# Kernel tuning notes

Measured on AMD Instinct MI355X. Metric: run time of the kernel, lower is better.

The kernel has to match this reference:

```python
import jax, jax.numpy as jnp
import numpy as np

B, H, C_LEN, Q_LEN = 64, 128, 1024, 128


def setup_inputs() -> dict:
    key = jax.random.key(0)
    k1, k2, k3 = jax.random.split(key, 3)
    context = jax.random.normal(k1, (B, H, C_LEN), dtype=jnp.float32)
    question = jax.random.normal(k2, (B, H, Q_LEN), dtype=jnp.float32)
    lim = np.sqrt(1.0 / H)
    w = jax.random.uniform(k3, (3 * H,), dtype=jnp.float32, minval=-lim, maxval=lim)
    return {"context": context, "question": question, "w": w}


def reference(context, question, w):
    # context: (B, H, C), question: (B, H, Q); w: (3H,) with cat order (q, c, cq)
    h = w.shape[0] // 3
    w_q, w_c, w_cq = w[:h], w[h:2 * h], w[2 * h:]
    c = jnp.transpose(context, (0, 2, 1))   # (B, C, H)
    q = jnp.transpose(question, (0, 2, 1))  # (B, Q, H)
    # trilinear similarity s[b,i,j] = c_i.w_c + q_j.w_q + (c_i*w_cq).q_j  -> (B, C, Q)
    s = (c @ w_c)[:, :, None] + (q @ w_q)[:, None, :] \
        + jnp.einsum('bih,bjh->bij', c * w_cq, q)
    # original applies softmax over dim=1 (context axis) for BOTH s1 and s2
    s1 = jax.nn.softmax(s, axis=1)           # (B, C, Q)
    a = jnp.einsum('bij,bjh->bih', s1, q)    # (B, C, H)
    l = jnp.einsum('bij,bkj->bik', s1, s1)   # (B, C, C)
    b = jnp.einsum('bik,bkh->bih', l, c)     # (B, C, H)
    out = jnp.concatenate([c, a, c * a, c * b], axis=2)  # (B, C, 4H)
    # dropout disabled (drop_prob=0) for deterministic reference
    return jnp.transpose(out, (0, 2, 1))     # (B, 4H, C)
```

## Files before the change

### kernel.cpp

```cpp
#include <hip/hip_runtime.h>

#define BB 64
#define HH 128
#define CC 1024
#define QQ 128

typedef unsigned short u16;
typedef unsigned int u32;
using bf16x8 = __attribute__((ext_vector_type(8))) short;
using f32x4 = __attribute__((ext_vector_type(4))) float;

#define MFMA16(a, b, c) __builtin_amdgcn_mfma_f32_16x16x32_bf16(a, b, c, 0, 0, 0)

__device__ __forceinline__ float lo2f(u32 u) {
  union { float f; u32 i; } v; v.i = u << 16; return v.f;
}
__device__ __forceinline__ float hi2f(u32 u) {
  union { float f; u32 i; } v; v.i = u & 0xFFFF0000u; return v.f;
}
__device__ __forceinline__ u16 f2b(float f) {
  union { float f; u32 i; } v; v.f = f;
  u32 r = v.i + 0x7FFFu + ((v.i >> 16) & 1u);
  return (u16)(r >> 16);
}
__device__ __forceinline__ u32 pack_hi2(float a, float b) {
  return (__float_as_uint(a) >> 16) | (__float_as_uint(b) & 0xFFFF0000u);
}
__device__ __forceinline__ u32 pack_lo2(float a, float b) {
  float ra = a - __uint_as_float(__float_as_uint(a) & 0xFFFF0000u);
  float rb = b - __uint_as_float(__float_as_uint(b) & 0xFFFF0000u);
  return (__float_as_uint(ra) >> 16) | (__float_as_uint(rb) & 0xFFFF0000u);
}

__device__ __forceinline__ void stage16(const float* __restrict__ p,
                                        u16* dhi, u16* dlo) {
  float4 a0 = *(const float4*)p;
  float4 a1 = *(const float4*)(p + 4);
  float4 a2 = *(const float4*)(p + 8);
  float4 a3 = *(const float4*)(p + 12);
  uint4 h0 = {pack_hi2(a0.x, a0.y), pack_hi2(a0.z, a0.w),
              pack_hi2(a1.x, a1.y), pack_hi2(a1.z, a1.w)};
  uint4 h1 = {pack_hi2(a2.x, a2.y), pack_hi2(a2.z, a2.w),
              pack_hi2(a3.x, a3.y), pack_hi2(a3.z, a3.w)};
  uint4 l0 = {pack_lo2(a0.x, a0.y), pack_lo2(a0.z, a0.w),
              pack_lo2(a1.x, a1.y), pack_lo2(a1.z, a1.w)};
  uint4 l1 = {pack_lo2(a2.x, a2.y), pack_lo2(a2.z, a2.w),
              pack_lo2(a3.x, a3.y), pack_lo2(a3.z, a3.w)};
  *(uint4*)dhi = h0;
  *(uint4*)(dhi + 8) = h1;
  *(uint4*)dlo = l0;
  *(uint4*)(dlo + 8) = l1;
}

__global__ __launch_bounds__(512) void k1_s_softmax(
    const float* __restrict__ ctx, const float* __restrict__ qst,
    const float* __restrict__ w, u16* __restrict__ s1ws,
    u16* __restrict__ s1tb) {
  const int b = blockIdx.x;
  const int j0 = blockIdx.y * 16;
  const int tid = threadIdx.x;
  const float* cb = ctx + (size_t)b * HH * CC;
  const float* qb = qst + (size_t)b * HH * QQ;

  float dotv[16][2];
  float qwq[16];
  float cwc[2] = {0.f, 0.f};
#pragma unroll
  for (int jj = 0; jj < 16; ++jj) {
    qwq[jj] = 0.f;
    dotv[jj][0] = dotv[jj][1] = 0.f;
  }

  for (int h = 0; h < HH; ++h) {
    const float2 cv = *(const float2*)(cb + (size_t)h * CC + tid * 2);
    float c0 = cv.x, c1 = cv.y;
    float wqv = w[h], wcv = w[HH + h], wcqv = w[2 * HH + h];
    cwc[0] += c0 * wcv; cwc[1] += c1 * wcv;
    float t0 = c0 * wcqv, t1 = c1 * wcqv;
    const float4* qrow = (const float4*)(qb + (size_t)h * QQ + j0);
    float4 q0 = qrow[0], q1 = qrow[1], q2 = qrow[2], q3 = qrow[3];
    float qv[16] = {q0.x, q0.y, q0.z, q0.w, q1.x, q1.y, q1.z, q1.w,
                    q2.x, q2.y, q2.z, q2.w, q3.x, q3.y, q3.z, q3.w};
#pragma unroll
    for (int jj = 0; jj < 16; ++jj) {
      qwq[jj] += qv[jj] * wqv;
      dotv[jj][0] += t0 * qv[jj];
      dotv[jj][1] += t1 * qv[jj];
    }
  }
#pragma unroll
  for (int jj = 0; jj < 16; ++jj) {
    float base = qwq[jj];
    dotv[jj][0] += cwc[0] + base;
    dotv[jj][1] += cwc[1] + base;
  }

  __shared__ float red[16 * 512];
  __shared__ float red2[16 * 32];
  __shared__ float bc[16];
  const int rj = tid >> 5, rs = tid & 31;

#pragma unroll
  for (int jj = 0; jj < 16; ++jj)
    red[jj * 512 + tid] = fmaxf(dotv[jj][0], dotv[jj][1]);
  __syncthreads();
  {
    float m = red[rj * 512 + rs * 16];
#pragma unroll
    for (int g = 1; g < 16; ++g) m = fmaxf(m, red[rj * 512 + rs * 16 + g]);
    red2[rj * 32 + rs] = m;
  }
  __syncthreads();
  if (tid < 16) {
    float m = red2[tid * 32];
#pragma unroll
    for (int g = 1; g < 32; ++g) m = fmaxf(m, red2[tid * 32 + g]);
    bc[tid] = m;
  }
  __syncthreads();

#pragma unroll
  for (int jj = 0; jj < 16; ++jj) {
    float mj = bc[jj];
    float e0 = __expf(dotv[jj][0] - mj);
    float e1 = __expf(dotv[jj][1] - mj);
    dotv[jj][0] = e0; dotv[jj][1] = e1;
    red[jj * 512 + tid] = e0 + e1;
  }
  __syncthreads();
  {
    float s = 0.f;
#pragma unroll
    for (int g = 0; g < 16; ++g) s += red[rj * 512 + rs * 16 + g];
    red2[rj * 32 + rs] = s;
  }
  __syncthreads();
  if (tid < 16) {
    float s = 0.f;
#pragma unroll
    for (int g = 0; g < 32; ++g) s += red2[tid * 32 + g];
    bc[tid] = 1.0f / s;
  }
  __syncthreads();

#pragma unroll
  for (int jj = 0; jj < 16; ++jj) {
    float inv = bc[jj];
    dotv[jj][0] *= inv;
    dotv[jj][1] *= inv;
  }
  u16* srow = s1ws + ((size_t)b * QQ + j0) * CC + tid * 2;
#pragma unroll
  for (int jj = 0; jj < 16; ++jj) {
    u32 pk = (u32)f2b(dotv[jj][0]) | ((u32)f2b(dotv[jj][1]) << 16);
    *(u32*)(srow + (size_t)jj * CC) = pk;
  }
  u16* stb = s1tb + (size_t)b * (16 * 1024 * 8);
  const int jg0 = j0 >> 3;
#pragma unroll
  for (int g = 0; g < 2; ++g) {
#pragma unroll
    for (int rr = 0; rr < 2; ++rr) {
      const int o = g * 8;
      uint4 v;
      v.x = (u32)f2b(dotv[o + 0][rr]) | ((u32)f2b(dotv[o + 1][rr]) << 16);
      v.y = (u32)f2b(dotv[o + 2][rr]) | ((u32)f2b(dotv[o + 3][rr]) << 16);
      v.z = (u32)f2b(dotv[o + 4][rr]) | ((u32)f2b(dotv[o + 5][rr]) << 16);
      v.w = (u32)f2b(dotv[o + 6][rr]) | ((u32)f2b(dotv[o + 7][rr]) << 16);
      *(uint4*)(stb + ((size_t)(jg0 + g) * 1024 + (tid * 2 + rr)) * 8) = v;
    }
  }
}

__global__ __launch_bounds__(256) void k2_t(
    const float* __restrict__ ctx, const u16* __restrict__ s1ws,
    float* __restrict__ tT) {
  const int b = blockIdx.x;
  const int h0 = (blockIdx.y >> 1) * 32;
  const int j0 = (blockIdx.y & 1) * 64;
  const int tid = threadIdx.x;
  const int lane = tid & 63;
  const int wv = tid >> 6;
  const int l15 = lane & 15, l4 = lane >> 4;

  __shared__ u16 sHi[32 * 136];
  __shared__ u16 sLo[32 * 136];

  f32x4 acc[2];
  acc[0] = 0.f; acc[1] = 0.f;

  const float* cb = ctx + ((size_t)b * HH + h0) * CC;
  const u16* sb = s1ws + ((size_t)b * QQ + j0 + wv * 16 + l15) * CC;
  const int srow = tid >> 3;
  const int scol = (tid & 7) * 16;

  for (int k0 = 0; k0 < CC; k0 += 128) {
    __syncthreads();
    stage16(cb + (size_t)srow * CC + k0 + scol,
            &sHi[srow * 136 + scol], &sLo[srow * 136 + scol]);
    __syncthreads();
#pragma unroll
    for (int kk = 0; kk < 4; ++kk) {
      bf16x8 bf = *(const bf16x8*)(sb + k0 + kk * 32 + l4 * 8);
#pragma unroll
      for (int ht = 0; ht < 2; ++ht) {
        const int ar = (ht * 16 + l15) * 136 + kk * 32 + l4 * 8;
        bf16x8 ah = *(const bf16x8*)&sHi[ar];
        bf16x8 al = *(const bf16x8*)&sLo[ar];
        acc[ht] = MFMA16(ah, bf, acc[ht]);
        acc[ht] = MFMA16(al, bf, acc[ht]);
      }
    }
  }
  float* tb = tT + (size_t)b * HH * QQ;
#pragma unroll
  for (int ht = 0; ht < 2; ++ht)
#pragma unroll
    for (int r = 0; r < 4; ++r)
      tb[(size_t)(h0 + ht * 16 + l4 * 4 + r) * QQ + j0 + wv * 16 + l15] =
          acc[ht][r];
}

__global__ __launch_bounds__(256, 2) void k3_out(
    const float* __restrict__ ctx, const float* __restrict__ qst,
    const u16* __restrict__ s1tb, const float* __restrict__ tT,
    float* __restrict__ out) {
  const int b = blockIdx.x;
  const int i0 = blockIdx.y * 128;
  const int tid = threadIdx.x;
  const int lane = tid & 63;
  const int wv = tid >> 6;
  const int l15 = lane & 15, l4 = lane >> 4;

  __shared__ u16 qHi[128 * 40], qLo[128 * 40];
  __shared__ u16 tHi[128 * 40], tLo[128 * 40];

  f32x4 accA[8][2], accB[8][2];
#pragma unroll
  for (int it = 0; it < 8; ++it)
#pragma unroll
    for (int ht = 0; ht < 2; ++ht) { accA[it][ht] = 0.f; accB[it][ht] = 0.f; }

  const u16* stb = s1tb + (size_t)b * (16 * 1024 * 8);
  const float* qb = qst + (size_t)b * HH * QQ;
  const float* tb = tT + (size_t)b * HH * QQ;
  const int srow = tid >> 1;
  const int scol = (tid & 1) * 16;

  for (int ks = 0; ks < 4; ++ks) {
    const int jb = ks * 32;
    __syncthreads();
    stage16(qb + (size_t)srow * QQ + jb + scol,
            &qHi[srow * 40 + scol], &qLo[srow * 40 + scol]);
    stage16(tb + (size_t)srow * QQ + jb + scol,
            &tHi[srow * 40 + scol], &tLo[srow * 40 + scol]);
    __syncthreads();
    bf16x8 qh[2], ql[2], th[2], tl[2];
#pragma unroll
    for (int ht = 0; ht < 2; ++ht) {
      const int ar = (wv * 32 + ht * 16 + l15) * 40 + l4 * 8;
      qh[ht] = *(const bf16x8*)&qHi[ar];
      ql[ht] = *(const bf16x8*)&qLo[ar];
      th[ht] = *(const bf16x8*)&tHi[ar];
      tl[ht] = *(const bf16x8*)&tLo[ar];
    }
#pragma unroll
    for (int half = 0; half < 2; ++half) {
      bf16x8 bfr[4];
#pragma unroll
      for (int t4 = 0; t4 < 4; ++t4) {
        const int it = half * 4 + t4;
        bfr[t4] = *(const bf16x8*)(stb +
            ((size_t)(ks * 4 + l4) * 1024 + i0 + it * 16 + l15) * 8);
      }
#pragma unroll
      for (int t4 = 0; t4 < 4; ++t4) {
        const int it = half * 4 + t4;
#pragma unroll
        for (int ht = 0; ht < 2; ++ht) {
          accA[it][ht] = MFMA16(qh[ht], bfr[t4], accA[it][ht]);
          accA[it][ht] = MFMA16(ql[ht], bfr[t4], accA[it][ht]);
          accB[it][ht] = MFMA16(th[ht], bfr[t4], accB[it][ht]);
          accB[it][ht] = MFMA16(tl[ht], bfr[t4], accB[it][ht]);
        }
      }
    }
  }

  const float* cb = ctx + (size_t)b * HH * CC;
  float* ob = out + (size_t)b * 4 * HH * CC;
#pragma unroll
  for (int it = 0; it < 8; ++it) {
    const int ii = i0 + it * 16 + l15;
#pragma unroll
    for (int ht = 0; ht < 2; ++ht) {
#pragma unroll
      for (int r = 0; r < 4; ++r) {
        const int h = wv * 32 + ht * 16 + l4 * 4 + r;
        const size_t base = (size_t)h * CC + ii;
        const float cv = cb[base];
        const float av = accA[it][ht][r];
        const float bv = accB[it][ht][r];
        ob[base] = cv;
        ob[(size_t)HH * CC + base] = av;
        ob[(size_t)2 * HH * CC + base] = cv * av;
        ob[(size_t)3 * HH * CC + base] = cv * bv;
      }
    }
  }
}

extern "C" void kernel_launch(void* const* d_in, const int* in_sizes, int n_in,
                              void* d_out, int out_size, void* d_ws, size_t ws_size,
                              hipStream_t stream) {
  const float* ctx = (const float*)d_in[0];
  const float* qst = (const float*)d_in[1];
  const float* w = (const float*)d_in[2];
  for (int k = 0; k < n_in; ++k) {
    if (in_sizes[k] == BB * HH * CC) ctx = (const float*)d_in[k];
    else if (in_sizes[k] == BB * HH * QQ) qst = (const float*)d_in[k];
    else if (in_sizes[k] == 3 * HH) w = (const float*)d_in[k];
  }
  float* out = (float*)d_out;

  u16* s1ws = (u16*)d_ws;
  u16* s1tb = (u16*)((char*)d_ws + (size_t)16 * 1024 * 1024);
  float* tT = (float*)((char*)d_ws + (size_t)32 * 1024 * 1024);

  k1_s_softmax<<<dim3(BB, QQ / 16), 512, 0, stream>>>(ctx, qst, w, s1ws, s1tb);
  k2_t<<<dim3(BB, 8), 256, 0, stream>>>(ctx, s1ws, tT);
  k3_out<<<dim3(BB, 8), 256, 0, stream>>>(ctx, qst, s1tb, tT, out);
}
```

Measured before the change: 250.9 us.

## Compute similarity scores with bf16 MFMA and prepacked transposed operands

Result: faster. 245.7 us (-2.1%).

```diff
diff --git a/kernel.cpp b/kernel.cpp
--- a/kernel.cpp
+++ b/kernel.cpp
@@ -12,12 +12,6 @@
 
 #define MFMA16(a, b, c) __builtin_amdgcn_mfma_f32_16x16x32_bf16(a, b, c, 0, 0, 0)
 
-__device__ __forceinline__ float lo2f(u32 u) {
-  union { float f; u32 i; } v; v.i = u << 16; return v.f;
-}
-__device__ __forceinline__ float hi2f(u32 u) {
-  union { float f; u32 i; } v; v.i = u & 0xFFFF0000u; return v.f;
-}
 __device__ __forceinline__ u16 f2b(float f) {
   union { float f; u32 i; } v; v.f = f;
   u32 r = v.i + 0x7FFFu + ((v.i >> 16) & 1u);
@@ -52,122 +46,212 @@
   *(uint4*)(dlo + 8) = l1;
 }
 
-__global__ __launch_bounds__(512) void k1_s_softmax(
-    const float* __restrict__ ctx, const float* __restrict__ qst,
-    const float* __restrict__ w, u16* __restrict__ s1ws,
+__global__ __launch_bounds__(256) void k_qw(
+    const float* __restrict__ qst, const float* __restrict__ w,
+    u16* __restrict__ qwh, u16* __restrict__ qwl) {
+  const int b = blockIdx.x;
+  const int tid = threadIdx.x;
+  __shared__ float ld[128 * 129];
+  __shared__ float wcq[128];
+  const float* qb = qst + (size_t)b * HH * QQ;
+#pragma unroll
+  for (int rep = 0; rep < 16; ++rep) {
+    int h = rep * 8 + (tid >> 5);
+    int jo = (tid & 31) * 4;
+    float4 v = *(const float4*)(qb + (size_t)h * QQ + jo);
+    float* d = &ld[h * 129 + jo];
+    d[0] = v.x; d[1] = v.y; d[2] = v.z; d[3] = v.w;
+  }
+  if (tid < 128) wcq[tid] = w[2 * HH + tid];
+  __syncthreads();
+  const int j = tid >> 1;
+  const int hh0 = (tid & 1) * 64;
+  u16* oh = qwh + (size_t)b * 144 * 128 + j * 128 + hh0;
+  u16* ol = qwl + (size_t)b * 144 * 128 + j * 128 + hh0;
+#pragma unroll
+  for (int g = 0; g < 8; ++g) {
+    u32 hw[4], lw[4];
+#pragma unroll
+    for (int p = 0; p < 4; ++p) {
+      int h = hh0 + g * 8 + p * 2;
+      float a = ld[h * 129 + j] * wcq[h];
+      float c = ld[(h + 1) * 129 + j] * wcq[h + 1];
+      hw[p] = pack_hi2(a, c);
+      lw[p] = pack_lo2(a, c);
+    }
+    uint4 vh = {hw[0], hw[1], hw[2], hw[3]};
+    uint4 vl = {lw[0], lw[1], lw[2], lw[3]};
+    *(uint4*)(oh + g * 8) = vh;
+    *(uint4*)(ol + g * 8) = vl;
+  }
+  if (tid < 128) {
+    int jr = 128 + (tid >> 3);
+    int hc = (tid & 7) * 16;
+    u32 hw[8], lw[8];
+#pragma unroll
+    for (int p = 0; p < 8; ++p) { hw[p] = 0; lw[p] = 0; }
+    if (jr == 128) {
+#pragma unroll
+      for (int p = 0; p < 8; ++p) {
+        float a = w[HH + hc + p * 2];
+        float c = w[HH + hc + p * 2 + 1];
+        hw[p] = pack_hi2(a, c);
+        lw[p] = pack_lo2(a, c);
+      }
+    }
+    u16* ph = qwh + (size_t)b * 144 * 128 + (size_t)jr * 128 + hc;
+    u16* pl = qwl + (size_t)b * 144 * 128 + (size_t)jr * 128 + hc;
+    uint4 vh0 = {hw[0], hw[1], hw[2], hw[3]};
+    uint4 vh1 = {hw[4], hw[5], hw[6], hw[7]};
+    uint4 vl0 = {lw[0], lw[1], lw[2], lw[3]};
+    uint4 vl1 = {lw[4], lw[5], lw[6], lw[7]};
+    *(uint4*)ph = vh0; *(uint4*)(ph + 8) = vh1;
+    *(uint4*)pl = vl0; *(uint4*)(pl + 8) = vl1;
+  }
+}
+
+__global__ __launch_bounds__(256) void k_ct(
+    const float* __restrict__ ctx, u16* __restrict__ cTh) {
+  const int b = blockIdx.x;
+  const int i0 = blockIdx.y * 128;
+  const int tid = threadIdx.x;
+  __shared__ float ld[128 * 129];
+  const float* cb = ctx + (size_t)b * HH * CC;
+#pragma unroll
+  for (int rep = 0; rep < 16; ++rep) {
+    int h = rep * 8 + (tid >> 5);
+    int io = (tid & 31) * 4;
+    float4 v = *(const float4*)(cb + (size_t)h * CC + i0 + io);
+    float* d = &ld[h * 129 + io];
+    d[0] = v.x; d[1] = v.y; d[2] = v.z; d[3] = v.w;
+  }
+  __syncthreads();
+  const int i = tid >> 1;
+  const int hh0 = (tid & 1) * 64;
+  u16* oh = cTh + (size_t)b * CC * HH + (size_t)(i0 + i) * 128 + hh0;
+#pragma unroll
+  for (int g = 0; g < 8; ++g) {
+    u32 hw[4];
+#pragma unroll
+    for (int p = 0; p < 4; ++p) {
+      int h = hh0 + g * 8 + p * 2;
+      hw[p] = pack_hi2(ld[h * 129 + i], ld[(h + 1) * 129 + i]);
+    }
+    uint4 vh = {hw[0], hw[1], hw[2], hw[3]};
+    *(uint4*)(oh + g * 8) = vh;
+  }
+}
+
+__global__ __launch_bounds__(512) void k0_softmax(
+    const u16* __restrict__ cTh, const u16* __restrict__ qwh,
+    const u16* __restrict__ qwl, u16* __restrict__ s1ws,
     u16* __restrict__ s1tb) {
   const int b = blockIdx.x;
   const int j0 = blockIdx.y * 16;
   const int tid = threadIdx.x;
-  const float* cb = ctx + (size_t)b * HH * CC;
-  const float* qb = qst + (size_t)b * HH * QQ;
-
-  float dotv[16][2];
-  float qwq[16];
-  float cwc[2] = {0.f, 0.f};
-#pragma unroll
-  for (int jj = 0; jj < 16; ++jj) {
-    qwq[jj] = 0.f;
-    dotv[jj][0] = dotv[jj][1] = 0.f;
-  }
-
-  for (int h = 0; h < HH; ++h) {
-    const float2 cv = *(const float2*)(cb + (size_t)h * CC + tid * 2);
-    float c0 = cv.x, c1 = cv.y;
-    float wqv = w[h], wcv = w[HH + h], wcqv = w[2 * HH + h];
-    cwc[0] += c0 * wcv; cwc[1] += c1 * wcv;
-    float t0 = c0 * wcqv, t1 = c1 * wcqv;
-    const float4* qrow = (const float4*)(qb + (size_t)h * QQ + j0);
-    float4 q0 = qrow[0], q1 = qrow[1], q2 = qrow[2], q3 = qrow[3];
-    float qv[16] = {q0.x, q0.y, q0.z, q0.w, q1.x, q1.y, q1.z, q1.w,
-                    q2.x, q2.y, q2.z, q2.w, q3.x, q3.y, q3.z, q3.w};
-#pragma unroll
-    for (int jj = 0; jj < 16; ++jj) {
-      qwq[jj] += qv[jj] * wqv;
-      dotv[jj][0] += t0 * qv[jj];
-      dotv[jj][1] += t1 * qv[jj];
-    }
-  }
-#pragma unroll
-  for (int jj = 0; jj < 16; ++jj) {
-    float base = qwq[jj];
-    dotv[jj][0] += cwc[0] + base;
-    dotv[jj][1] += cwc[1] + base;
-  }
-
-  __shared__ float red[16 * 512];
-  __shared__ float red2[16 * 32];
-  __shared__ float bc[16];
-  const int rj = tid >> 5, rs = tid & 31;
-
-#pragma unroll
-  for (int jj = 0; jj < 16; ++jj)
-    red[jj * 512 + tid] = fmaxf(dotv[jj][0], dotv[jj][1]);
+  const int lane = tid & 63;
+  const int wv = tid >> 6;
+  const int l15 = lane & 15, l4 = lane >> 4;
+  __shared__ float wred[2][8][4][4];
+
+  const u16* cb = cTh + (size_t)b * CC * HH;
+  const u16* qhp = qwh + (size_t)b * 144 * 128;
+  const u16* qlp = qwl + (size_t)b * 144 * 128;
+
+  bf16x8 aqh[4], aql[4], axh[4];
+#pragma unroll
+  for (int kk = 0; kk < 4; ++kk) {
+    const int off = kk * 32 + l4 * 8;
+    aqh[kk] = *(const bf16x8*)(qhp + (size_t)(j0 + l15) * 128 + off);
+    aql[kk] = *(const bf16x8*)(qlp + (size_t)(j0 + l15) * 128 + off);
+    axh[kk] = *(const bf16x8*)(qhp + (size_t)(128 + l15) * 128 + off);
+  }
+
+  f32x4 sv[8];
+  float cwcv[8];
+#pragma unroll
+  for (int it = 0; it < 8; ++it) {
+    const int i = wv * 128 + it * 16 + l15;
+    f32x4 aR = {0.f, 0.f, 0.f, 0.f};
+    f32x4 aX = {0.f, 0.f, 0.f, 0.f};
+#pragma unroll
+    for (int kk = 0; kk < 4; ++kk) {
+      bf16x8 bh = *(const bf16x8*)(cb + (size_t)i * 128 + kk * 32 + l4 * 8);
+      aR = MFMA16(aqh[kk], bh, aR);
+      aR = MFMA16(aql[kk], bh, aR);
+      aX = MFMA16(axh[kk], bh, aX);
+    }
+    cwcv[it] = __shfl(aX[0], l15);
+    sv[it] = aR;
+  }
+#pragma unroll
+  for (int it = 0; it < 8; ++it)
+#pragma unroll
+    for (int r = 0; r < 4; ++r) sv[it][r] += cwcv[it];
+
+  float mj[4];
+#pragma unroll
+  for (int r = 0; r < 4; ++r) {
+    float m = sv[0][r];
+#pragma unroll
+    for (int it = 1; it < 8; ++it) m = fmaxf(m, sv[it][r]);
+#pragma unroll
+    for (int msk = 1; msk < 16; msk <<= 1) m = fmaxf(m, __shfl_xor(m, msk));
+    mj[r] = m;
+  }
+  if (l15 == 0) {
+#pragma unroll
+    for (int r = 0; r < 4; ++r) wred[0][wv][l4][r] = mj[r];
+  }
   __syncthreads();
-  {
-    float m = red[rj * 512 + rs * 16];
-#pragma unroll
-    for (int g = 1; g < 16; ++g) m = fmaxf(m, red[rj * 512 + rs * 16 + g]);
-    red2[rj * 32 + rs] = m;
+  float gm[4];
+#pragma unroll
+  for (int r = 0; r < 4; ++r) {
+    float m = wred[0][0][l4][r];
+#pragma unroll
+    for (int w2 = 1; w2 < 8; ++w2) m = fmaxf(m, wred[0][w2][l4][r]);
+    gm[r] = m;
+  }
+
+#pragma unroll
+  for (int it = 0; it < 8; ++it)
+#pragma unroll
+    for (int r = 0; r < 4; ++r) sv[it][r] = __expf(sv[it][r] - gm[r]);
+  float sj[4];
+#pragma unroll
+  for (int r = 0; r < 4; ++r) {
+    float s = 0.f;
+#pragma unroll
+    for (int it = 0; it < 8; ++it) s += sv[it][r];
+#pragma unroll
+    for (int msk = 1; msk < 16; msk <<= 1) s += __shfl_xor(s, msk);
+    sj[r] = s;
+  }
+  if (l15 == 0) {
+#pragma unroll
+    for (int r = 0; r < 4; ++r) wred[1][wv][l4][r] = sj[r];
   }
   __syncthreads();
-  if (tid < 16) {
-    float m = red2[tid * 32];
-#pragma unroll
-    for (int g = 1; g < 32; ++g) m = fmaxf(m, red2[tid * 32 + g]);
-    bc[tid] = m;
-  }
-  __syncthreads();
-
-#pragma unroll
-  for (int jj = 0; jj < 16; ++jj) {
-    float mj = bc[jj];
-    float e0 = __expf(dotv[jj][0] - mj);
-    float e1 = __expf(dotv[jj][1] - mj);
-    dotv[jj][0] = e0; dotv[jj][1] = e1;
-    red[jj * 512 + tid] = e0 + e1;
-  }
-  __syncthreads();
-  {
+  float inv_[4];
+#pragma unroll
+  for (int r = 0; r < 4; ++r) {
     float s = 0.f;
 #pragma unroll
-    for (int g = 0; g < 16; ++g) s += red[rj * 512 + rs * 16 + g];
-    red2[rj * 32 + rs] = s;
-  }
-  __syncthreads();
-  if (tid < 16) {
-    float s = 0.f;
-#pragma unroll
-    for (int g = 0; g < 32; ++g) s += red2[tid * 32 + g];
-    bc[tid] = 1.0f / s;
-  }
-  __syncthreads();
-
-#pragma unroll
-  for (int jj = 0; jj < 16; ++jj) {
-    float inv = bc[jj];
-    dotv[jj][0] *= inv;
-    dotv[jj][1] *= inv;
-  }
-  u16* srow = s1ws + ((size_t)b * QQ + j0) * CC + tid * 2;
-#pragma unroll
-  for (int jj = 0; jj < 16; ++jj) {
-    u32 pk = (u32)f2b(dotv[jj][0]) | ((u32)f2b(dotv[jj][1]) << 16);
-    *(u32*)(srow + (size_t)jj * CC) = pk;
-  }
-  u16* stb = s1tb + (size_t)b * (16 * 1024 * 8);
-  const int jg0 = j0 >> 3;
-#pragma unroll
-  for (int g = 0; g < 2; ++g) {
-#pragma unroll
-    for (int rr = 0; rr < 2; ++rr) {
-      const int o = g * 8;
-      uint4 v;
-      v.x = (u32)f2b(dotv[o + 0][rr]) | ((u32)f2b(dotv[o + 1][rr]) << 16);
-      v.y = (u32)f2b(dotv[o + 2][rr]) | ((u32)f2b(dotv[o + 3][rr]) << 16);
-      v.z = (u32)f2b(dotv[o + 4][rr]) | ((u32)f2b(dotv[o + 5][rr]) << 16);
-      v.w = (u32)f2b(dotv[o + 6][rr]) | ((u32)f2b(dotv[o + 7][rr]) << 16);
-      *(uint4*)(stb + ((size_t)(jg0 + g) * 1024 + (tid * 2 + rr)) * 8) = v;
+    for (int w2 = 0; w2 < 8; ++w2) s += wred[1][w2][l4][r];
+    inv_[r] = 1.0f / s;
+  }
+
+  u16* ws = s1ws + (size_t)b * QQ * CC;
+  u16* tb = s1tb + (size_t)b * (16 * 1024 * 8);
+#pragma unroll
+  for (int it = 0; it < 8; ++it) {
+    const int i = wv * 128 + it * 16 + l15;
+#pragma unroll
+    for (int r = 0; r < 4; ++r) {
+      const int j = j0 + l4 * 4 + r;
+      u16 pv = f2b(sv[it][r] * inv_[r]);
+      ws[(size_t)j * CC + i] = pv;
+      tb[((size_t)(j >> 3) * 1024 + i) * 8 + (j & 7)] = pv;
     }
   }
 }
@@ -327,7 +411,14 @@
   u16* s1tb = (u16*)((char*)d_ws + (size_t)16 * 1024 * 1024);
   float* tT = (float*)((char*)d_ws + (size_t)32 * 1024 * 1024);
 
-  k1_s_softmax<<<dim3(BB, QQ / 16), 512, 0, stream>>>(ctx, qst, w, s1ws, s1tb);
+  char* ob = (char*)d_out;
+  u16* qwl = (u16*)(ob + 112721920);
+  u16* qwh = (u16*)(ob + 115081216);
+  u16* cTh = (u16*)(ob + 117440512);
+
+  k_qw<<<BB, 256, 0, stream>>>(qst, w, qwh, qwl);
+  k_ct<<<dim3(BB, 8), 256, 0, stream>>>(ctx, cTh);
+  k0_softmax<<<dim3(BB, 8), 512, 0, stream>>>(cTh, qwh, qwl, s1ws, s1tb);
   k2_t<<<dim3(BB, 8), 256, 0, stream>>>(ctx, s1ws, tT);
   k3_out<<<dim3(BB, 8), 256, 0, stream>>>(ctx, qst, s1tb, tT, out);
 }
```
